# Kernel optimization log

Hardware: AMD Instinct MI355X
Metric: run time of the kernel (lower is better)

Reference implementation:

```python
import jax, jax.numpy as jnp
import numpy as np
import math

B, N, IN_DIM, HID, OUT = 16, 1024, 3, 32, 4
RATIO = 0.2
K1 = math.ceil(RATIO * N)    # 205 nodes kept after pool 1
K2 = math.ceil(RATIO * K1)   # 41 nodes kept after pool 2
AVG_DEG = 16.0
BN_EPS = 1e-5


def setup_inputs() -> dict:
    key = jax.random.key(0)
    ks = jax.random.split(key, 16)
    x = jax.random.normal(ks[0], (B, N, IN_DIM), jnp.float32)
    # sparse random undirected adjacency (binary edge weights = 1), no self loops
    u = jax.random.uniform(ks[1], (B, N, N))
    A = (u < (AVG_DEG / N)).astype(jnp.float32)
    A = jnp.maximum(A, jnp.swapaxes(A, -1, -2))
    A = A * (1.0 - jnp.eye(N, dtype=jnp.float32))
    g = lambda i, shp: (jax.random.normal(ks[i], shp, jnp.float32) * 0.1)
    params = dict(
        Wd0=g(2, (IN_DIM, HID)), bd0=jnp.zeros((HID,), jnp.float32),
        Wd1=g(3, (HID, HID)),    bd1=jnp.zeros((HID,), jnp.float32),
        Wd2=g(4, (HID, HID)),    bd2=jnp.zeros((HID,), jnp.float32),
        Wu0=g(5, (HID, HID)),    bu0=jnp.zeros((HID,), jnp.float32),
        Wu1=g(6, (HID, HID)),    bu1=jnp.zeros((HID,), jnp.float32),
        p1=g(7, (HID,)), p2=g(8, (HID,)),
        gamma=jnp.ones((HID,), jnp.float32), beta=jnp.zeros((HID,), jnp.float32),
        W1=g(9, (HID, HID)),  b1=jnp.zeros((HID,), jnp.float32),
        W2=g(10, (HID, HID)), b2=jnp.zeros((HID,), jnp.float32),
        W3=g(11, (HID, OUT)), b3=jnp.zeros((OUT,), jnp.float32),
    )
    return {"x": x, "adj": A, **params}


def _gcn(A, x, W, b):
    # GCNConv(improved=True): A_hat = A + 2I, symmetric normalization
    n = A.shape[-1]
    A_hat = A + 2.0 * jnp.eye(n, dtype=A.dtype)
    deg = A_hat.sum(-1)                              # [B, n]
    dis = jnp.where(deg > 0, jax.lax.rsqrt(deg), 0.0)
    A_norm = dis[..., :, None] * A_hat * dis[..., None, :]
    return jnp.einsum('bij,bjf->bif', A_norm, x @ W) + b


def _augment(A):
    # GraphUNet.augment_adj: add self loops (w=1), square adjacency, drop diag
    n = A.shape[-1]
    eye = jnp.eye(n, dtype=A.dtype)
    Bm = A + eye
    A2 = jnp.einsum('bij,bjk->bik', Bm, Bm)
    return A2 * (1.0 - eye)


def _topk_pool(A, x, p, k):
    # TopKPooling: score = tanh(x.p / ||p||), keep top-k nodes per graph
    score = jnp.tanh((x @ p) / jnp.linalg.norm(p))   # [B, n]
    vals, perm = jax.lax.top_k(score, k)             # descending, matches PyG
    bidx = jnp.arange(x.shape[0])[:, None]
    x_p = x[bidx, perm] * vals[..., None]
    A_p = A[bidx[..., None], perm[:, :, None], perm[:, None, :]]
    return A_p, x_p, perm


def reference(x, adj, Wd0, bd0, Wd1, bd1, Wd2, bd2, Wu0, bu0, Wu1, bu1,
              p1, p2, gamma, beta, W1, b1, W2, b2, W3, b3):
    bidx = jnp.arange(x.shape[0])[:, None]
    # ---- GraphUNet down path ----
    h0 = jax.nn.relu(_gcn(adj, x, Wd0, bd0))
    A1, h, perm1 = _topk_pool(_augment(adj), h0, p1, K1)
    h1 = jax.nn.relu(_gcn(A1, h, Wd1, bd1))
    A2, h, perm2 = _topk_pool(_augment(A1), h1, p2, K2)
    h = jax.nn.relu(_gcn(A2, h, Wd2, bd2))
    # ---- up path (sum_res=True) ----
    up = jnp.zeros_like(h1).at[bidx, perm2].set(h)
    h = jax.nn.relu(_gcn(A1, h1 + up, Wu0, bu0))
    up = jnp.zeros_like(h0).at[bidx, perm1].set(h)
    h = _gcn(adj, h0 + up, Wu1, bu1)   # last up conv: no activation
    # ---- BatchNorm1d over all nodes (training-mode batch stats, biased var) ----
    mean = h.mean((0, 1))
    var = h.var((0, 1))
    hn = (h - mean) * jax.lax.rsqrt(var + BN_EPS) * gamma + beta
    # ---- outnetwork MLP (dropout = identity in eval), LeakyReLU slope 0.01 ----
    r = jax.nn.leaky_relu(hn @ W1 + b1)
    r = jax.nn.leaky_relu(r @ W2 + b2)
    r = r @ W3 + b3
    return r.at[..., 0].set(jax.nn.sigmoid(r[..., 0]))
```

## Files before the change

### kernel.cpp

```cpp
#include <hip/hip_runtime.h>
#include <cmath>

#define BB 16
#define NN 1024
#define KK1 205
#define KK2 42
#define CAP 96

__global__ void k_deg_csr(const float* __restrict__ adj, float* __restrict__ dis0,
                          int* __restrict__ ncnt, int* __restrict__ nbr,
                          unsigned long long* __restrict__ mask) {
  int row = blockIdx.x * 4 + (threadIdx.x >> 6);
  int lane = threadIdx.x & 63;
  const float* ar = adj + (size_t)row * NN;
  int base = 0;
  for (int c = 0; c < 16; ++c) {
    float v = ar[c * 64 + lane];
    unsigned long long m = __ballot(v != 0.0f);
    if (lane == c) mask[(size_t)row * 16 + c] = m;
    if (v != 0.0f) {
      int pos = base + __popcll(m & ((1ull << lane) - 1ull));
      if (pos < CAP) nbr[(size_t)row * CAP + pos] = c * 64 + lane;
    }
    base += __popcll(m);
  }
  if (lane == 0) {
    ncnt[row] = base < CAP ? base : CAP;
    dis0[row] = rsqrtf((float)base + 2.0f);
  }
}

__global__ void k_xw3(const float* __restrict__ x, const float* __restrict__ W,
                      const float* __restrict__ dis, float* __restrict__ out) {
  int idx = blockIdx.x * 256 + threadIdx.x;
  int f = idx & 31; int node = idx >> 5;
  const float* xr = x + (size_t)node * 3;
  float s = xr[0] * W[f] + xr[1] * W[32 + f] + xr[2] * W[64 + f];
  out[idx] = s * dis[node];
}

__global__ void k_xw32(const float* __restrict__ in, const float* __restrict__ W,
                       const float* __restrict__ dis, float* __restrict__ out) {
  int idx = blockIdx.x * 256 + threadIdx.x;
  int f = idx & 31; int node = idx >> 5;
  const float* xr = in + (size_t)node * 32;
  float s = 0.f;
#pragma unroll
  for (int k = 0; k < 32; ++k) s += xr[k] * W[k * 32 + f];
  out[idx] = s * dis[node];
}

template<bool RELU>
__global__ void k_spmm(const float* __restrict__ dxw, const float* __restrict__ dis,
                       const int* __restrict__ ncnt, const int* __restrict__ nbr,
                       const float* __restrict__ bias, float* __restrict__ out) {
  int tid = threadIdx.x;
  int g = tid >> 5, f = tid & 31;
  int node = blockIdx.x * 8 + g;
  int b = node >> 10;
  int cnt = ncnt[node];
  const int* lst = nbr + (size_t)node * CAP;
  float acc = 0.f;
  for (int k = 0; k < cnt; ++k) {
    int j = lst[k];
    acc += dxw[(size_t)((b << 10) + j) * 32 + f];
  }
  acc += 2.0f * dxw[(size_t)node * 32 + f];
  float r = dis[node] * acc + bias[f];
  if (RELU) r = fmaxf(r, 0.f);
  out[(size_t)node * 32 + f] = r;
}

template<int MPAD>
__global__ void k_topk(const float* __restrict__ h, const float* __restrict__ p,
                       int M, int K, int* __restrict__ perm, float* __restrict__ vals) {
  __shared__ unsigned long long skey[MPAD];
  int b = blockIdx.x, t = threadIdx.x;
  float nn = 0.f;
#pragma unroll
  for (int k = 0; k < 32; ++k) nn += p[k] * p[k];
  unsigned int ordv;
  if (t < M) {
    const float* hr = h + (size_t)(b * M + t) * 32;
    float d = 0.f;
#pragma unroll
    for (int k = 0; k < 32; ++k) d += hr[k] * p[k];
    float v = tanhf(d / sqrtf(nn));
    unsigned int u = __float_as_uint(v);
    if (u == 0x80000000u) u = 0u;
    ordv = (u & 0x80000000u) ? ~u : (u | 0x80000000u);
  } else {
    ordv = 0u;
  }
  skey[t] = ((unsigned long long)(~ordv) << 32) | (unsigned int)t;
  __syncthreads();
  for (int k = 2; k <= MPAD; k <<= 1) {
    for (int j = k >> 1; j > 0; j >>= 1) {
      int ixj = t ^ j;
      if (ixj > t) {
        unsigned long long a = skey[t], c = skey[ixj];
        bool up = ((t & k) == 0);
        if (up == (a > c)) { skey[t] = c; skey[ixj] = a; }
      }
      __syncthreads();
    }
  }
  if (t < K) {
    unsigned long long kk = skey[t];
    unsigned int ord = ~(unsigned int)(kk >> 32);
    unsigned int u = (ord & 0x80000000u) ? (ord & 0x7FFFFFFFu) : ~ord;
    perm[b * K + t] = (int)(kk & 0xFFFFFFFFull);
    vals[b * K + t] = __uint_as_float(u);
  }
}

__global__ void k_gather(const float* __restrict__ h, const int* __restrict__ perm,
                         const float* __restrict__ vals, int M, int K,
                         float* __restrict__ hp) {
  int idx = blockIdx.x * 256 + threadIdx.x;
  int f = idx & 31; int q = idx >> 5;
  int k = q % K, b = q / K;
  int src = perm[b * K + k];
  hp[idx] = h[(size_t)(b * M + src) * 32 + f] * vals[b * K + k];
}

__global__ void k_buildA1(const unsigned long long* __restrict__ mask,
                          const int* __restrict__ perm1, float* __restrict__ A1,
                          float* __restrict__ dis1) {
  __shared__ unsigned long long smT[16 * KK1];
  __shared__ int sp[KK1];
  int blk = blockIdx.x;
  int b = blk / 52, chunk = blk - b * 52;
  int t = threadIdx.x;
  if (t < KK1) sp[t] = perm1[b * KK1 + t];
  __syncthreads();
  for (int q = t; q < KK1 * 16; q += 256) {
    int i = q >> 4, w = q & 15;
    smT[w * KK1 + i] = mask[((size_t)(b * NN + sp[i])) * 16 + w];
  }
  __syncthreads();
  int wave = t >> 6, lane = t & 63;
  int i = chunk * 4 + wave;
  if (i < KK1) {
    unsigned long long r[16];
#pragma unroll
    for (int w = 0; w < 16; ++w) r[w] = smT[w * KK1 + i];
    float rowsum = 0.f;
    for (int j = lane; j < KK1; j += 64) {
      int cnt = 0;
#pragma unroll
      for (int w = 0; w < 16; ++w) cnt += __popcll(r[w] & smT[w * KK1 + j]);
      int pj = sp[j];
      float edge = (float)((r[pj >> 6] >> (pj & 63)) & 1ull);
      float v = (j == i) ? 0.f : ((float)cnt + 2.f * edge);
      A1[((size_t)(b * KK1) + i) * KK1 + j] = v;
      rowsum += v;
    }
#pragma unroll
    for (int o = 32; o; o >>= 1) rowsum += __shfl_xor(rowsum, o);
    if (lane == 0) dis1[b * KK1 + i] = rsqrtf(rowsum + 2.0f);
  }
}

template<bool RELU>
__global__ __launch_bounds__(256) void k_dense_apply(
    const float* __restrict__ A, const float* __restrict__ t,
    const float* __restrict__ dis, const float* __restrict__ bias,
    int M, float* __restrict__ out) {
  int row = blockIdx.x;
  int b = row / M, i = row - b * M;
  int tid = threadIdx.x;
  int g = tid >> 5, f = tid & 31;
  const float* Ar = A + (size_t)row * M;
  const float* tb = t + (size_t)b * M * 32;
  float acc = 0.f;
  for (int j = g; j < M; j += 8)
    acc += Ar[j] * tb[j * 32 + f];
  __shared__ float ls[8][32];
  ls[g][f] = acc;
  __syncthreads();
  if (tid < 32) {
    float s = 0.f;
#pragma unroll
    for (int q = 0; q < 8; ++q) s += ls[q][tid];
    s += 2.0f * tb[i * 32 + tid];
    float r = dis[row] * s + bias[tid];
    if (RELU) r = fmaxf(r, 0.f);
    out[(size_t)row * 32 + tid] = r;
  }
}

__global__ void k_buildA2(const float* __restrict__ A1, const int* __restrict__ perm2,
                          float* __restrict__ A2, float* __restrict__ dis2) {
  __shared__ float gsum[8];
  int row = blockIdx.x;
  int b = row / KK2, i = row - b * KK2;
  int g = threadIdx.x >> 5, lane = threadIdx.x & 31;
  int pi = perm2[b * KK2 + i];
  const float* Ri = A1 + ((size_t)(b * KK1 + pi)) * KK1;
  float part = 0.f;
  for (int j = g; j < KK2; j += 8) {
    int pj = perm2[b * KK2 + j];
    const float* Rj = A1 + ((size_t)(b * KK1 + pj)) * KK1;
    float s = 0.f;
    for (int k = lane; k < KK1; k += 32) s += Ri[k] * Rj[k];
#pragma unroll
    for (int o = 16; o; o >>= 1) s += __shfl_xor(s, o, 32);
    float v = (i == j) ? 0.f : (s + 2.0f * Ri[pj]);
    if (lane == 0) {
      A2[((size_t)(b * KK2) + i) * KK2 + j] = v;
      part += v;
    }
  }
  if (lane == 0) gsum[g] = part;
  __syncthreads();
  if (threadIdx.x == 0) {
    float s = 0.f;
#pragma unroll
    for (int q = 0; q < 8; ++q) s += gsum[q];
    dis2[row] = rsqrtf(s + 2.0f);
  }
}

__global__ void k_copy(const float* __restrict__ in, float* __restrict__ out) {
  int idx = blockIdx.x * 256 + threadIdx.x;
  out[idx] = in[idx];
}
__global__ void k_scatter_add(const float* __restrict__ src, const int* __restrict__ perm,
                              int K, int Mdst, float* __restrict__ dst) {
  int idx = blockIdx.x * 256 + threadIdx.x;
  int f = idx & 31; int q = idx >> 5;
  int k = q % K, b = q / K;
  int d = perm[b * K + k];
  dst[((size_t)(b * Mdst) + d) * 32 + f] += src[idx];
}

__global__ void k_bnstats(const float* __restrict__ h, float* __restrict__ acc) {
  int t = threadIdx.x;
  int f = t & 31, g = t >> 5;
  int rowBase = blockIdx.x * 128;
  float s = 0.f, sq = 0.f;
  for (int r = g; r < 128; r += 8) {
    float v = h[(size_t)(rowBase + r) * 32 + f];
    s += v; sq += v * v;
  }
  __shared__ float ls[8][32], lq[8][32];
  ls[g][f] = s; lq[g][f] = sq;
  __syncthreads();
  if (t < 32) {
    float S = 0.f, Q = 0.f;
#pragma unroll
    for (int i = 0; i < 8; ++i) { S += ls[i][t]; Q += lq[i][t]; }
    atomicAdd(&acc[t], S);
    atomicAdd(&acc[32 + t], Q);
  }
}

__global__ __launch_bounds__(64) void k_mlp(
    const float* __restrict__ h, const float* __restrict__ acc,
    const float* __restrict__ gamma, const float* __restrict__ beta,
    const float* __restrict__ W1, const float* __restrict__ b1,
    const float* __restrict__ W2, const float* __restrict__ b2,
    const float* __restrict__ W3, const float* __restrict__ b3,
    float* __restrict__ out) {
  __shared__ float sW1[1024], sW2[1024], sW3[128];
  __shared__ float sb1[32], sb2[32], sb3[4], sscale[32], sshift[32];
  int t = threadIdx.x;
  {
    const float4* W1v = (const float4*)W1; float4* d1 = (float4*)sW1;
#pragma unroll
    for (int i = 0; i < 4; ++i) d1[t + i * 64] = W1v[t + i * 64];
    const float4* W2v = (const float4*)W2; float4* d2 = (float4*)sW2;
#pragma unroll
    for (int i = 0; i < 4; ++i) d2[t + i * 64] = W2v[t + i * 64];
    if (t < 32) ((float4*)sW3)[t] = ((const float4*)W3)[t];
    if (t < 32) { sb1[t] = b1[t]; sb2[t] = b2[t]; }
    if (t < 4) sb3[t] = b3[t];
    if (t < 32) {
      const float inv = 1.0f / (float)(BB * NN);
      float m = acc[t] * inv;
      float v = acc[32 + t] * inv - m * m;
      float sc = gamma[t] * rsqrtf(v + 1e-5f);
      sscale[t] = sc;
      sshift[t] = beta[t] - m * sc;
    }
  }
  __syncthreads();
  int node = blockIdx.x * 64 + t;
  const float4* hr = (const float4*)(h + (size_t)node * 32);
  float hn[32];
#pragma unroll
  for (int i = 0; i < 8; ++i) {
    float4 x = hr[i];
    hn[i * 4 + 0] = x.x * sscale[i * 4 + 0] + sshift[i * 4 + 0];
    hn[i * 4 + 1] = x.y * sscale[i * 4 + 1] + sshift[i * 4 + 1];
    hn[i * 4 + 2] = x.z * sscale[i * 4 + 2] + sshift[i * 4 + 2];
    hn[i * 4 + 3] = x.w * sscale[i * 4 + 3] + sshift[i * 4 + 3];
  }
  float r1[32];
#pragma unroll
  for (int f = 0; f < 32; ++f) r1[f] = sb1[f];
#pragma unroll
  for (int k = 0; k < 32; ++k) {
    float a = hn[k];
#pragma unroll
    for (int f = 0; f < 32; ++f) r1[f] += a * sW1[k * 32 + f];
  }
#pragma unroll
  for (int f = 0; f < 32; ++f) r1[f] = r1[f] > 0.f ? r1[f] : 0.01f * r1[f];
  float r2[32];
#pragma unroll
  for (int f = 0; f < 32; ++f) r2[f] = sb2[f];
#pragma unroll
  for (int k = 0; k < 32; ++k) {
    float a = r1[k];
#pragma unroll
    for (int f = 0; f < 32; ++f) r2[f] += a * sW2[k * 32 + f];
  }
#pragma unroll
  for (int f = 0; f < 32; ++f) r2[f] = r2[f] > 0.f ? r2[f] : 0.01f * r2[f];
  float r3[4];
#pragma unroll
  for (int c = 0; c < 4; ++c) r3[c] = sb3[c];
#pragma unroll
  for (int k = 0; k < 32; ++k) {
    float a = r2[k];
#pragma unroll
    for (int c = 0; c < 4; ++c) r3[c] += a * sW3[k * 4 + c];
  }
  float4 o;
  o.x = 1.0f / (1.0f + expf(-r3[0]));
  o.y = r3[1]; o.z = r3[2]; o.w = r3[3];
  ((float4*)out)[node] = o;
}

extern "C" void kernel_launch(void* const* d_in, const int* in_sizes, int n_in,
                              void* d_out, int out_size, void* d_ws, size_t ws_size,
                              hipStream_t stream) {
  const float* x    = (const float*)d_in[0];
  const float* adj  = (const float*)d_in[1];
  const float* Wd0  = (const float*)d_in[2];
  const float* bd0  = (const float*)d_in[3];
  const float* Wd1  = (const float*)d_in[4];
  const float* bd1  = (const float*)d_in[5];
  const float* Wd2  = (const float*)d_in[6];
  const float* bd2  = (const float*)d_in[7];
  const float* Wu0  = (const float*)d_in[8];
  const float* bu0  = (const float*)d_in[9];
  const float* Wu1  = (const float*)d_in[10];
  const float* bu1  = (const float*)d_in[11];
  const float* p1   = (const float*)d_in[12];
  const float* p2   = (const float*)d_in[13];
  const float* gamma= (const float*)d_in[14];
  const float* beta = (const float*)d_in[15];
  const float* W1   = (const float*)d_in[16];
  const float* b1   = (const float*)d_in[17];
  const float* W2   = (const float*)d_in[18];
  const float* b2   = (const float*)d_in[19];
  const float* W3   = (const float*)d_in[20];
  const float* b3   = (const float*)d_in[21];
  float* out = (float*)d_out;

  char* w = (char*)d_ws;
  auto alloc = [&](size_t bytes) -> void* {
    void* p = (void*)w;
    w += (bytes + 255) & ~(size_t)255;
    return p;
  };
  float* dis0 = (float*)alloc(BB * NN * 4);
  int*   ncnt = (int*)alloc(BB * NN * 4);
  int*   nbr  = (int*)alloc((size_t)BB * NN * CAP * 4);
  unsigned long long* mask = (unsigned long long*)alloc((size_t)BB * NN * 16 * 8);
  float* dxw  = (float*)alloc((size_t)BB * NN * 32 * 4);
  float* h0   = (float*)alloc((size_t)BB * NN * 32 * 4);
  int*   perm1= (int*)alloc(BB * KK1 * 4);
  float* vals1= (float*)alloc(BB * KK1 * 4);
  float* hp1  = (float*)alloc((size_t)BB * KK1 * 32 * 4);
  float* A1   = (float*)alloc((size_t)BB * KK1 * KK1 * 4);
  float* dis1 = (float*)alloc(BB * KK1 * 4);
  float* t1   = (float*)alloc((size_t)BB * KK1 * 32 * 4);
  float* h1   = (float*)alloc((size_t)BB * KK1 * 32 * 4);
  int*   perm2= (int*)alloc(BB * KK2 * 4);
  float* vals2= (float*)alloc(BB * KK2 * 4);
  float* hp2  = (float*)alloc((size_t)BB * KK2 * 32 * 4);
  float* A2   = (float*)alloc((size_t)BB * KK2 * KK2 * 4);
  float* dis2 = (float*)alloc(BB * KK2 * 4);
  float* t2   = (float*)alloc((size_t)BB * KK2 * 32 * 4);
  float* h2   = (float*)alloc((size_t)BB * KK2 * 32 * 4);
  float* u1   = (float*)alloc((size_t)BB * KK1 * 32 * 4);
  float* hu0  = (float*)alloc((size_t)BB * KK1 * 32 * 4);
  float* u0   = (float*)alloc((size_t)BB * NN * 32 * 4);
  float* hfin = (float*)alloc((size_t)BB * NN * 32 * 4);
  float* bnacc= (float*)alloc(64 * 4);

  const int TOT_N32  = BB * NN * 32;
  const int TOT_K132 = BB * KK1 * 32;
  const int TOT_K232 = BB * KK2 * 32;

  k_deg_csr<<<BB * NN / 4, 256, 0, stream>>>(adj, dis0, ncnt, nbr, mask);
  k_xw3<<<TOT_N32 / 256, 256, 0, stream>>>(x, Wd0, dis0, dxw);
  k_spmm<true><<<BB * NN / 8, 256, 0, stream>>>(dxw, dis0, ncnt, nbr, bd0, h0);
  k_topk<1024><<<BB, 1024, 0, stream>>>(h0, p1, NN, KK1, perm1, vals1);
  k_gather<<<TOT_K132 / 256, 256, 0, stream>>>(h0, perm1, vals1, NN, KK1, hp1);
  k_buildA1<<<BB * 52, 256, 0, stream>>>(mask, perm1, A1, dis1);
  k_xw32<<<TOT_K132 / 256, 256, 0, stream>>>(hp1, Wd1, dis1, t1);
  k_dense_apply<true><<<BB * KK1, 256, 0, stream>>>(A1, t1, dis1, bd1, KK1, h1);
  k_topk<256><<<BB, 256, 0, stream>>>(h1, p2, KK1, KK2, perm2, vals2);
  k_gather<<<TOT_K232 / 256, 256, 0, stream>>>(h1, perm2, vals2, KK1, KK2, hp2);
  k_buildA2<<<BB * KK2, 256, 0, stream>>>(A1, perm2, A2, dis2);
  k_xw32<<<TOT_K232 / 256, 256, 0, stream>>>(hp2, Wd2, dis2, t2);
  k_dense_apply<true><<<BB * KK2, 256, 0, stream>>>(A2, t2, dis2, bd2, KK2, h2);
  k_copy<<<TOT_K132 / 256, 256, 0, stream>>>(h1, u1);
  k_scatter_add<<<TOT_K232 / 256, 256, 0, stream>>>(h2, perm2, KK2, KK1, u1);
  k_xw32<<<TOT_K132 / 256, 256, 0, stream>>>(u1, Wu0, dis1, t1);
  k_dense_apply<true><<<BB * KK1, 256, 0, stream>>>(A1, t1, dis1, bu0, KK1, hu0);
  k_copy<<<TOT_N32 / 256, 256, 0, stream>>>(h0, u0);
  k_scatter_add<<<TOT_K132 / 256, 256, 0, stream>>>(hu0, perm1, KK1, NN, u0);
  k_xw32<<<TOT_N32 / 256, 256, 0, stream>>>(u0, Wu1, dis0, dxw);
  k_spmm<false><<<BB * NN / 8, 256, 0, stream>>>(dxw, dis0, ncnt, nbr, bu1, hfin);
  hipMemsetAsync(bnacc, 0, 64 * sizeof(float), stream);
  k_bnstats<<<128, 256, 0, stream>>>(hfin, bnacc);
  k_mlp<<<BB * NN / 64, 64, 0, stream>>>(hfin, bnacc, gamma, beta,
                                         W1, b1, W2, b2, W3, b3, out);
}
```

Measured before the change: 343.1 us.

## Fuse gather, scatter-add and feature transforms into adjacent kernels

Folds the first x@W transform into the degree/CSR kernel and the top-k gather into the following feature transform. The up-path copy+scatter_add is replaced by an inverse-permutation map written in top-k, so the transform reads h plus the pooled result directly. It also replaces the BN atomics and memset with per-block partials reduced in the MLP kernel, and unrolls the SpMM neighbor loop into four accumulators with int4 index loads. These changes drop about seven launches and several intermediate buffers. The cost is extra indirection and a serial 128-entry reduction inside each MLP block.

```diff
diff --git a/kernel.cpp b/kernel.cpp
--- a/kernel.cpp
+++ b/kernel.cpp
@@ -7,9 +7,11 @@
 #define KK2 42
 #define CAP 96
 
-__global__ void k_deg_csr(const float* __restrict__ adj, float* __restrict__ dis0,
-                          int* __restrict__ ncnt, int* __restrict__ nbr,
-                          unsigned long long* __restrict__ mask) {
+__global__ void k_deg_csr(const float* __restrict__ adj, const float* __restrict__ x,
+                          const float* __restrict__ W,
+                          float* __restrict__ dis0, int* __restrict__ ncnt,
+                          int* __restrict__ nbr, unsigned long long* __restrict__ mask,
+                          float* __restrict__ dxw) {
   int row = blockIdx.x * 4 + (threadIdx.x >> 6);
   int lane = threadIdx.x & 63;
   const float* ar = adj + (size_t)row * NN;
@@ -24,30 +26,16 @@
     }
     base += __popcll(m);
   }
+  float dis = rsqrtf((float)base + 2.0f);
   if (lane == 0) {
     ncnt[row] = base < CAP ? base : CAP;
-    dis0[row] = rsqrtf((float)base + 2.0f);
-  }
-}
-
-__global__ void k_xw3(const float* __restrict__ x, const float* __restrict__ W,
-                      const float* __restrict__ dis, float* __restrict__ out) {
-  int idx = blockIdx.x * 256 + threadIdx.x;
-  int f = idx & 31; int node = idx >> 5;
-  const float* xr = x + (size_t)node * 3;
-  float s = xr[0] * W[f] + xr[1] * W[32 + f] + xr[2] * W[64 + f];
-  out[idx] = s * dis[node];
-}
-
-__global__ void k_xw32(const float* __restrict__ in, const float* __restrict__ W,
-                       const float* __restrict__ dis, float* __restrict__ out) {
-  int idx = blockIdx.x * 256 + threadIdx.x;
-  int f = idx & 31; int node = idx >> 5;
-  const float* xr = in + (size_t)node * 32;
-  float s = 0.f;
-#pragma unroll
-  for (int k = 0; k < 32; ++k) s += xr[k] * W[k * 32 + f];
-  out[idx] = s * dis[node];
+    dis0[row] = dis;
+  }
+  if (lane < 32) {
+    float x0 = x[row * 3], x1 = x[row * 3 + 1], x2 = x[row * 3 + 2];
+    float s = x0 * W[lane] + x1 * W[32 + lane] + x2 * W[64 + lane];
+    dxw[(size_t)row * 32 + lane] = s * dis;
+  }
 }
 
 template<bool RELU>
@@ -60,11 +48,18 @@
   int b = node >> 10;
   int cnt = ncnt[node];
   const int* lst = nbr + (size_t)node * CAP;
-  float acc = 0.f;
-  for (int k = 0; k < cnt; ++k) {
-    int j = lst[k];
-    acc += dxw[(size_t)((b << 10) + j) * 32 + f];
-  }
+  const float* dbase = dxw + ((size_t)(b << 10) << 5);
+  float a0 = 0.f, a1 = 0.f, a2 = 0.f, a3 = 0.f;
+  int k = 0;
+  for (; k + 4 <= cnt; k += 4) {
+    int4 j4 = *(const int4*)(lst + k);
+    a0 += dbase[(size_t)j4.x * 32 + f];
+    a1 += dbase[(size_t)j4.y * 32 + f];
+    a2 += dbase[(size_t)j4.z * 32 + f];
+    a3 += dbase[(size_t)j4.w * 32 + f];
+  }
+  for (; k < cnt; ++k) a0 += dbase[(size_t)lst[k] * 32 + f];
+  float acc = (a0 + a1) + (a2 + a3);
   acc += 2.0f * dxw[(size_t)node * 32 + f];
   float r = dis[node] * acc + bias[f];
   if (RELU) r = fmaxf(r, 0.f);
@@ -73,7 +68,8 @@
 
 template<int MPAD>
 __global__ void k_topk(const float* __restrict__ h, const float* __restrict__ p,
-                       int M, int K, int* __restrict__ perm, float* __restrict__ vals) {
+                       int M, int K, int* __restrict__ perm, float* __restrict__ vals,
+                       int* __restrict__ inv) {
   __shared__ unsigned long long skey[MPAD];
   int b = blockIdx.x, t = threadIdx.x;
   float nn = 0.f;
@@ -89,6 +85,7 @@
     unsigned int u = __float_as_uint(v);
     if (u == 0x80000000u) u = 0u;
     ordv = (u & 0x80000000u) ? ~u : (u | 0x80000000u);
+    inv[b * M + t] = -1;
   } else {
     ordv = 0u;
   }
@@ -109,19 +106,11 @@
     unsigned long long kk = skey[t];
     unsigned int ord = ~(unsigned int)(kk >> 32);
     unsigned int u = (ord & 0x80000000u) ? (ord & 0x7FFFFFFFu) : ~ord;
-    perm[b * K + t] = (int)(kk & 0xFFFFFFFFull);
+    int idx = (int)(kk & 0xFFFFFFFFull);
+    perm[b * K + t] = idx;
     vals[b * K + t] = __uint_as_float(u);
-  }
-}
-
-__global__ void k_gather(const float* __restrict__ h, const int* __restrict__ perm,
-                         const float* __restrict__ vals, int M, int K,
-                         float* __restrict__ hp) {
-  int idx = blockIdx.x * 256 + threadIdx.x;
-  int f = idx & 31; int q = idx >> 5;
-  int k = q % K, b = q / K;
-  int src = perm[b * K + k];
-  hp[idx] = h[(size_t)(b * M + src) * 32 + f] * vals[b * K + k];
+    inv[b * M + idx] = t;
+  }
 }
 
 __global__ void k_buildA1(const unsigned long long* __restrict__ mask,
@@ -160,6 +149,42 @@
     for (int o = 32; o; o >>= 1) rowsum += __shfl_xor(rowsum, o);
     if (lane == 0) dis1[b * KK1 + i] = rsqrtf(rowsum + 2.0f);
   }
+}
+
+__global__ void k_xw32g(const float* __restrict__ h, const int* __restrict__ perm,
+                        const float* __restrict__ vals, const float* __restrict__ W,
+                        const float* __restrict__ dis, int M, int K,
+                        float* __restrict__ out) {
+  int idx = blockIdx.x * 256 + threadIdx.x;
+  int f = idx & 31; int q = idx >> 5;
+  int b = q / K;
+  int src = perm[q];
+  const float* xr = h + (size_t)(b * M + src) * 32;
+  float s = 0.f;
+#pragma unroll
+  for (int k = 0; k < 32; ++k) s += xr[k] * W[k * 32 + f];
+  out[idx] = s * dis[q] * vals[q];
+}
+
+__global__ void k_xw32u(const float* __restrict__ h, const float* __restrict__ up,
+                        const int* __restrict__ inv, const float* __restrict__ W,
+                        const float* __restrict__ dis, int M, int K,
+                        float* __restrict__ out) {
+  int idx = blockIdx.x * 256 + threadIdx.x;
+  int f = idx & 31; int node = idx >> 5;
+  int b = node / M;
+  int iv = inv[node];
+  const float* xr = h + (size_t)node * 32;
+  float s = 0.f;
+  if (iv >= 0) {
+    const float* ur = up + (size_t)(b * K + iv) * 32;
+#pragma unroll
+    for (int k = 0; k < 32; ++k) s += (xr[k] + ur[k]) * W[k * 32 + f];
+  } else {
+#pragma unroll
+    for (int k = 0; k < 32; ++k) s += xr[k] * W[k * 32 + f];
+  }
+  out[idx] = s * dis[node];
 }
 
 template<bool RELU>
@@ -222,20 +247,7 @@
   }
 }
 
-__global__ void k_copy(const float* __restrict__ in, float* __restrict__ out) {
-  int idx = blockIdx.x * 256 + threadIdx.x;
-  out[idx] = in[idx];
-}
-__global__ void k_scatter_add(const float* __restrict__ src, const int* __restrict__ perm,
-                              int K, int Mdst, float* __restrict__ dst) {
-  int idx = blockIdx.x * 256 + threadIdx.x;
-  int f = idx & 31; int q = idx >> 5;
-  int k = q % K, b = q / K;
-  int d = perm[b * K + k];
-  dst[((size_t)(b * Mdst) + d) * 32 + f] += src[idx];
-}
-
-__global__ void k_bnstats(const float* __restrict__ h, float* __restrict__ acc) {
+__global__ void k_bnstats(const float* __restrict__ h, float* __restrict__ pacc) {
   int t = threadIdx.x;
   int f = t & 31, g = t >> 5;
   int rowBase = blockIdx.x * 128;
@@ -251,13 +263,13 @@
     float S = 0.f, Q = 0.f;
 #pragma unroll
     for (int i = 0; i < 8; ++i) { S += ls[i][t]; Q += lq[i][t]; }
-    atomicAdd(&acc[t], S);
-    atomicAdd(&acc[32 + t], Q);
+    pacc[blockIdx.x * 64 + t] = S;
+    pacc[blockIdx.x * 64 + 32 + t] = Q;
   }
 }
 
 __global__ __launch_bounds__(64) void k_mlp(
-    const float* __restrict__ h, const float* __restrict__ acc,
+    const float* __restrict__ h, const float* __restrict__ pacc,
     const float* __restrict__ gamma, const float* __restrict__ beta,
     const float* __restrict__ W1, const float* __restrict__ b1,
     const float* __restrict__ W2, const float* __restrict__ b2,
@@ -277,9 +289,11 @@
     if (t < 32) { sb1[t] = b1[t]; sb2[t] = b2[t]; }
     if (t < 4) sb3[t] = b3[t];
     if (t < 32) {
+      float S = 0.f, Q = 0.f;
+      for (int q = 0; q < 128; ++q) { S += pacc[q * 64 + t]; Q += pacc[q * 64 + 32 + t]; }
       const float inv = 1.0f / (float)(BB * NN);
-      float m = acc[t] * inv;
-      float v = acc[32 + t] * inv - m * m;
+      float m = S * inv;
+      float v = Q * inv - m * m;
       float sc = gamma[t] * rsqrtf(v + 1e-5f);
       sscale[t] = sc;
       sshift[t] = beta[t] - m * sc;
@@ -375,51 +389,41 @@
   float* h0   = (float*)alloc((size_t)BB * NN * 32 * 4);
   int*   perm1= (int*)alloc(BB * KK1 * 4);
   float* vals1= (float*)alloc(BB * KK1 * 4);
-  float* hp1  = (float*)alloc((size_t)BB * KK1 * 32 * 4);
+  int*   inv1 = (int*)alloc(BB * NN * 4);
   float* A1   = (float*)alloc((size_t)BB * KK1 * KK1 * 4);
   float* dis1 = (float*)alloc(BB * KK1 * 4);
   float* t1   = (float*)alloc((size_t)BB * KK1 * 32 * 4);
   float* h1   = (float*)alloc((size_t)BB * KK1 * 32 * 4);
   int*   perm2= (int*)alloc(BB * KK2 * 4);
   float* vals2= (float*)alloc(BB * KK2 * 4);
-  float* hp2  = (float*)alloc((size_t)BB * KK2 * 32 * 4);
+  int*   inv2 = (int*)alloc(BB * KK1 * 4);
   float* A2   = (float*)alloc((size_t)BB * KK2 * KK2 * 4);
   float* dis2 = (float*)alloc(BB * KK2 * 4);
   float* t2   = (float*)alloc((size_t)BB * KK2 * 32 * 4);
   float* h2   = (float*)alloc((size_t)BB * KK2 * 32 * 4);
-  float* u1   = (float*)alloc((size_t)BB * KK1 * 32 * 4);
   float* hu0  = (float*)alloc((size_t)BB * KK1 * 32 * 4);
-  float* u0   = (float*)alloc((size_t)BB * NN * 32 * 4);
   float* hfin = (float*)alloc((size_t)BB * NN * 32 * 4);
-  float* bnacc= (float*)alloc(64 * 4);
+  float* pacc = (float*)alloc(128 * 64 * 4);
 
   const int TOT_N32  = BB * NN * 32;
   const int TOT_K132 = BB * KK1 * 32;
   const int TOT_K232 = BB * KK2 * 32;
 
-  k_deg_csr<<<BB * NN / 4, 256, 0, stream>>>(adj, dis0, ncnt, nbr, mask);
-  k_xw3<<<TOT_N32 / 256, 256, 0, stream>>>(x, Wd0, dis0, dxw);
+  k_deg_csr<<<BB * NN / 4, 256, 0, stream>>>(adj, x, Wd0, dis0, ncnt, nbr, mask, dxw);
   k_spmm<true><<<BB * NN / 8, 256, 0, stream>>>(dxw, dis0, ncnt, nbr, bd0, h0);
-  k_topk<1024><<<BB, 1024, 0, stream>>>(h0, p1, NN, KK1, perm1, vals1);
-  k_gather<<<TOT_K132 / 256, 256, 0, stream>>>(h0, perm1, vals1, NN, KK1, hp1);
+  k_topk<1024><<<BB, 1024, 0, stream>>>(h0, p1, NN, KK1, perm1, vals1, inv1);
   k_buildA1<<<BB * 52, 256, 0, stream>>>(mask, perm1, A1, dis1);
-  k_xw32<<<TOT_K132 / 256, 256, 0, stream>>>(hp1, Wd1, dis1, t1);
+  k_xw32g<<<TOT_K132 / 256, 256, 0, stream>>>(h0, perm1, vals1, Wd1, dis1, NN, KK1, t1);
   k_dense_apply<true><<<BB * KK1, 256, 0, stream>>>(A1, t1, dis1, bd1, KK1, h1);
-  k_topk<256><<<BB, 256, 0, stream>>>(h1, p2, KK1, KK2, perm2, vals2);
-  k_gather<<<TOT_K232 / 256, 256, 0, stream>>>(h1, perm2, vals2, KK1, KK2, hp2);
+  k_topk<256><<<BB, 256, 0, stream>>>(h1, p2, KK1, KK2, perm2, vals2, inv2);
   k_buildA2<<<BB * KK2, 256, 0, stream>>>(A1, perm2, A2, dis2);
-  k_xw32<<<TOT_K232 / 256, 256, 0, stream>>>(hp2, Wd2, dis2, t2);
+  k_xw32g<<<TOT_K232 / 256, 256, 0, stream>>>(h1, perm2, vals2, Wd2, dis2, KK1, KK2, t2);
   k_dense_apply<true><<<BB * KK2, 256, 0, stream>>>(A2, t2, dis2, bd2, KK2, h2);
-  k_copy<<<TOT_K132 / 256, 256, 0, stream>>>(h1, u1);
-  k_scatter_add<<<TOT_K232 / 256, 256, 0, stream>>>(h2, perm2, KK2, KK1, u1);
-  k_xw32<<<TOT_K132 / 256, 256, 0, stream>>>(u1, Wu0, dis1, t1);
+  k_xw32u<<<TOT_K132 / 256, 256, 0, stream>>>(h1, h2, inv2, Wu0, dis1, KK1, KK2, t1);
   k_dense_apply<true><<<BB * KK1, 256, 0, stream>>>(A1, t1, dis1, bu0, KK1, hu0);
-  k_copy<<<TOT_N32 / 256, 256, 0, stream>>>(h0, u0);
-  k_scatter_add<<<TOT_K132 / 256, 256, 0, stream>>>(hu0, perm1, KK1, NN, u0);
-  k_xw32<<<TOT_N32 / 256, 256, 0, stream>>>(u0, Wu1, dis0, dxw);
+  k_xw32u<<<TOT_N32 / 256, 256, 0, stream>>>(h0, hu0, inv1, Wu1, dis0, NN, KK1, dxw);
   k_spmm<false><<<BB * NN / 8, 256, 0, stream>>>(dxw, dis0, ncnt, nbr, bu1, hfin);
-  hipMemsetAsync(bnacc, 0, 64 * sizeof(float), stream);
-  k_bnstats<<<128, 256, 0, stream>>>(hfin, bnacc);
-  k_mlp<<<BB * NN / 64, 64, 0, stream>>>(hfin, bnacc, gamma, beta,
+  k_bnstats<<<128, 256, 0, stream>>>(hfin, pacc);
+  k_mlp<<<BB * NN / 64, 64, 0, stream>>>(hfin, pacc, gamma, beta,
                                          W1, b1, W2, b2, W3, b3, out);
 }
```

New measurement: 304.3 us. 11.3% less time.
